# Kernel optimization log

Hardware: AMD Instinct MI355X
Metric: run time of the kernel (lower is better)

Reference implementation:

```python
import jax, jax.numpy as jnp
import numpy as np
from jax import lax

C = 16        # channel_n
HID = 128     # hidden_size
IC = 3        # input_channels (kept fixed each step)
STEPS = 32
FIRE_RATE = 0.5


def setup_inputs() -> dict:
    key = jax.random.key(0)
    k0, k1, k2, k3, k4 = jax.random.split(key, 5)
    B, H, W = 8, 256, 256
    x = jax.random.normal(k0, (B, C, H, W), jnp.float32)
    # depthwise 3x3 kernels, HWIO layout with I=1 (feature_group_count=C)
    w_p0 = jax.random.normal(k1, (3, 3, 1, C), jnp.float32) * 0.1
    w_p1 = jax.random.normal(k2, (3, 3, 1, C), jnp.float32) * 0.1
    # 1x1 conv MLP: fc0 [3C -> HID] (with bias), fc1 [HID -> C] (no bias)
    w_fc0 = jax.random.normal(k3, (3 * C, HID), jnp.float32) / np.sqrt(3.0 * C)
    b_fc0 = jnp.zeros((HID,), jnp.float32)
    # NOTE: original zero-inits fc1 (dx would be identically 0); use small
    # random weights so the baseline exercises nontrivial math.
    w_fc1 = jax.random.normal(k4, (HID, C), jnp.float32) * (0.1 / np.sqrt(HID))
    return {"x": x, "w_p0": w_p0, "w_p1": w_p1, "w_fc0": w_fc0,
            "b_fc0": b_fc0, "w_fc1": w_fc1}


def _dwconv3x3_reflect(x, w):
    # x: [B,H,W,C], w: [3,3,1,C]; reflect pad then depthwise VALID conv
    xp = jnp.pad(x, ((0, 0), (1, 1), (1, 1), (0, 0)), mode='reflect')
    return lax.conv_general_dilated(
        xp, w, window_strides=(1, 1), padding='VALID',
        dimension_numbers=('NHWC', 'HWIO', 'NHWC'), feature_group_count=C)


def reference(x, w_p0, w_p1, w_fc0, b_fc0, w_fc1):
    x = jnp.transpose(x, (0, 2, 3, 1))  # NCHW -> NHWC [B,H,W,C]
    img = x                              # input_image clone
    B, H, W, _ = x.shape
    keys = jax.random.split(jax.random.key(42), STEPS)

    def step(xc, k):
        perc = jnp.concatenate(
            [xc, _dwconv3x3_reflect(xc, w_p0), _dwconv3x3_reflect(xc, w_p1)],
            axis=-1)                                         # [B,H,W,3C]
        h = jax.nn.relu(jnp.einsum('bhwc,cd->bhwd', perc, w_fc0) + b_fc0)
        dx = jnp.einsum('bhwd,dc->bhwc', h, w_fc1)           # [B,H,W,C]
        mask = (jax.random.uniform(k, (B, H, W, 1)) <= FIRE_RATE).astype(xc.dtype)
        xn = xc + dx * mask
        # first IC channels hold the input image, kept fixed each step
        xn = jnp.concatenate([img[..., :IC], xn[..., IC:]], axis=-1)
        return xn, None

    x_final, _ = lax.scan(step, x, keys)
    x_final = jnp.transpose(x_final, (0, 3, 1, 2))  # NHWC -> NCHW
    out = x_final[:, 3:4, :, :]
    return out, x_final
```

## Files before the change

### kernel.cpp

```cpp
#include <hip/hip_runtime.h>
#include <stdint.h>

#define Cc   16
#define HIDD 128
#define Bn   8
#define Hh   256
#define Ww   256
#define HW   (Hh * Ww)
#define NPIX (Bn * HW)
#define NSTEPS 32

typedef _Float16 half8 __attribute__((ext_vector_type(8)));
typedef float floatx16 __attribute__((ext_vector_type(16)));

__host__ __device__ inline void threefry2x32(uint32_t k1, uint32_t k2,
                                             uint32_t x0, uint32_t x1,
                                             uint32_t& o0, uint32_t& o1) {
  const uint32_t ks2 = k1 ^ k2 ^ 0x1BD11BDAu;
  uint32_t v0 = x0 + k1;
  uint32_t v1 = x1 + k2;
#define ROTL32(x, n) (((x) << (n)) | ((x) >> (32 - (n))))
#define R4(a, b, c, d)                                    \
  { v0 += v1; v1 = ROTL32(v1, a); v1 ^= v0;               \
    v0 += v1; v1 = ROTL32(v1, b); v1 ^= v0;               \
    v0 += v1; v1 = ROTL32(v1, c); v1 ^= v0;               \
    v0 += v1; v1 = ROTL32(v1, d); v1 ^= v0; }
  R4(13, 15, 26, 6)   v0 += k2;  v1 += ks2 + 1u;
  R4(17, 29, 16, 24)  v0 += ks2; v1 += k1 + 2u;
  R4(13, 15, 26, 6)   v0 += k1;  v1 += k2 + 3u;
  R4(17, 29, 16, 24)  v0 += k2;  v1 += ks2 + 4u;
  R4(13, 15, 26, 6)   v0 += ks2; v1 += k1 + 5u;
#undef R4
#undef ROTL32
  o0 = v0;
  o1 = v1;
}

__device__ inline uint32_t pk2(_Float16 a, _Float16 b) {
  union { _Float16 h[2]; uint32_t u; } t;
  t.h[0] = a; t.h[1] = b;
  return t.u;
}
__device__ inline half8 mk8(uint32_t a, uint32_t b, uint32_t c, uint32_t d) {
  union { uint32_t u[4]; half8 h; } t;
  t.u[0] = a; t.u[1] = b; t.u[2] = c; t.u[3] = d;
  return t.h;
}

__global__ __launch_bounds__(256) void k_prep(const float* __restrict__ wfc0,
                                              const float* __restrict__ wfc1,
                                              unsigned short* __restrict__ wf) {
  const int idx = blockIdx.x * 256 + threadIdx.x;
  if (idx < 12288) {
    const int j = idx & 7;
    const int t = idx >> 3;
    const int lane = t & 63;
    const int t2 = t >> 6;
    const int spl = t2 & 1;
    const int fk = t2 >> 1;
    const int kt = fk % 3;
    const int Mt = fk / 3;
    const int m = Mt * 32 + (lane & 31);
    const int k = kt * 16 + (lane >> 5) * 8 + j;
    const float v = wfc0[k * HIDD + m];
    const _Float16 hi = (_Float16)v;
    const _Float16 r = spl ? (_Float16)(v - (float)hi) : hi;
    union { _Float16 h; unsigned short s; } cv; cv.h = r;
    wf[idx] = cv.s;
  } else if (idx < 20480) {
    const int idx2 = idx - 12288;
    const int j = idx2 & 7;
    const int t = idx2 >> 3;
    const int lane = t & 63;
    const int t2 = t >> 6;
    const int spl = t2 & 1;
    const int kt2 = t2 >> 1;
    const int m = lane & 31;
    const int k = kt2 * 16 + (lane >> 5) * 8 + j;
    const float v = (m < 13) ? wfc1[k * 16 + (m + 3)] : 0.f;
    const _Float16 hi = (_Float16)v;
    const _Float16 r = spl ? (_Float16)(v - (float)hi) : hi;
    union { _Float16 h; unsigned short s; } cv; cv.h = r;
    wf[idx] = cv.s;
  }
}

__global__ __launch_bounds__(256) void k_nchw_to_nhwc(const float* __restrict__ x,
                                                      float* __restrict__ st) {
  const int p = blockIdx.x * 256 + threadIdx.x;
  const int b = p >> 16;
  const int hw = p & 65535;
  const float* src = x + (size_t)b * (Cc * HW) + hw;
  float v[16];
#pragma unroll
  for (int c = 0; c < 16; c++) v[c] = src[(size_t)c * HW];
  float4* dst = (float4*)(st + (size_t)p * 16);
#pragma unroll
  for (int q = 0; q < 4; q++)
    dst[q] = make_float4(v[4 * q], v[4 * q + 1], v[4 * q + 2], v[4 * q + 3]);
}

__global__ __launch_bounds__(256) void k_step(const float* __restrict__ in,
                                              float* __restrict__ out,
                                              const float* __restrict__ wp0,
                                              const float* __restrict__ wp1,
                                              const unsigned short* __restrict__ wf,
                                              const float* __restrict__ bfc0,
                                              uint32_t key0, uint32_t key1) {
  __shared__ __align__(16) unsigned short s_wf[20480];
  __shared__ __align__(16) float s_bias[128];

  const int tid = threadIdx.x;
  {
    const uint4* src = (const uint4*)wf;
    uint4* dst = (uint4*)s_wf;
#pragma unroll
    for (int i = 0; i < 10; i++) dst[tid + 256 * i] = src[tid + 256 * i];
    if (tid < 32) ((float4*)s_bias)[tid] = ((const float4*)bfc0)[tid];
  }
  __syncthreads();

  const int lane = tid & 63;
  const int h8 = (tid >> 5) & 1;
  const int ln31 = tid & 31;
  const int wv = tid >> 6;
  const uint32_t wbase = ((uint32_t)blockIdx.x << 8) + (uint32_t)wv * 64u;

  const int b = blockIdx.x >> 8;
  const int h = blockIdx.x & 255;
  const int w = tid;
  const int rows[3] = { (h == 0) ? 1 : h - 1, h, (h == 255) ? 254 : h + 1 };
  const int cols[3] = { (w == 0) ? 1 : w - 1, w, (w == 255) ? 254 : w + 1 };

  float perc[48];
#pragma unroll
  for (int i = 16; i < 48; i++) perc[i] = 0.f;

#pragma unroll
  for (int ty = 0; ty < 3; ty++) {
#pragma unroll
    for (int tx = 0; tx < 3; tx++) {
      const int tap = ty * 3 + tx;
      const float4* pv =
          (const float4*)(in + (size_t)(((b << 8) + rows[ty]) * 256 + cols[tx]) * 16);
#pragma unroll
      for (int q = 0; q < 4; q++) {
        float4 v = pv[q];
        float vv[4] = { v.x, v.y, v.z, v.w };
#pragma unroll
        for (int j = 0; j < 4; j++) {
          const int c = 4 * q + j;
          perc[16 + c] = fmaf(wp0[tap * 16 + c], vv[j], perc[16 + c]);
          perc[32 + c] = fmaf(wp1[tap * 16 + c], vv[j], perc[32 + c]);
          if (tap == 4) perc[c] = vv[j];
        }
      }
    }
  }

  uint32_t hi2[24], lo2[24];
#pragma unroll
  for (int q = 0; q < 24; q++) {
    const float a = perc[2 * q], bq = perc[2 * q + 1];
    const _Float16 ah = (_Float16)a, bh = (_Float16)bq;
    const _Float16 al = (_Float16)(a - (float)ah), bl = (_Float16)(bq - (float)bh);
    hi2[q] = pk2(ah, bh);
    lo2[q] = pk2(al, bl);
  }

  uint32_t B0h[3][4], B0l[3][4], B1h[3][4], B1l[3][4];
#pragma unroll
  for (int kt = 0; kt < 3; kt++) {
#pragma unroll
    for (int d = 0; d < 4; d++) {
      const uint32_t olh = hi2[kt * 8 + d], ohh = hi2[kt * 8 + 4 + d];
      const uint32_t pl_h = __shfl_xor(olh, 32, 64);
      const uint32_t ph_h = __shfl_xor(ohh, 32, 64);
      B0h[kt][d] = h8 ? ph_h : olh;
      B1h[kt][d] = h8 ? ohh : pl_h;
      const uint32_t oll = lo2[kt * 8 + d], ohl = lo2[kt * 8 + 4 + d];
      const uint32_t pl_l = __shfl_xor(oll, 32, 64);
      const uint32_t ph_l = __shfl_xor(ohl, 32, 64);
      B0l[kt][d] = h8 ? ph_l : oll;
      B1l[kt][d] = h8 ? ohl : pl_l;
    }
  }

  floatx16 g2a, g2b;
#pragma unroll
  for (int i = 0; i < 16; i++) { g2a[i] = 0.f; g2b[i] = 0.f; }

#pragma unroll
  for (int Mt = 0; Mt < 4; Mt++) {
    half8 Ah[3], Al[3];
#pragma unroll
    for (int kt = 0; kt < 3; kt++) {
      Ah[kt] = *(const half8*)&s_wf[((Mt * 3 + kt) * 2 + 0) * 512 + lane * 8];
      Al[kt] = *(const half8*)&s_wf[((Mt * 3 + kt) * 2 + 1) * 512 + lane * 8];
    }
    const float4 bb0 = *(const float4*)&s_bias[Mt * 32 + 4 * h8];
    const float4 bb1 = *(const float4*)&s_bias[Mt * 32 + 8 + 4 * h8];
    const float4 bb2 = *(const float4*)&s_bias[Mt * 32 + 16 + 4 * h8];
    const float4 bb3 = *(const float4*)&s_bias[Mt * 32 + 24 + 4 * h8];
    floatx16 acc0 = { bb0.x, bb0.y, bb0.z, bb0.w, bb1.x, bb1.y, bb1.z, bb1.w,
                      bb2.x, bb2.y, bb2.z, bb2.w, bb3.x, bb3.y, bb3.z, bb3.w };
    floatx16 acc1 = acc0;

#pragma unroll
    for (int kt = 0; kt < 3; kt++) {
      const half8 b0h = mk8(B0h[kt][0], B0h[kt][1], B0h[kt][2], B0h[kt][3]);
      const half8 b0l = mk8(B0l[kt][0], B0l[kt][1], B0l[kt][2], B0l[kt][3]);
      const half8 b1h = mk8(B1h[kt][0], B1h[kt][1], B1h[kt][2], B1h[kt][3]);
      const half8 b1l = mk8(B1l[kt][0], B1l[kt][1], B1l[kt][2], B1l[kt][3]);
      acc0 = __builtin_amdgcn_mfma_f32_32x32x16_f16(Ah[kt], b0h, acc0, 0, 0, 0);
      acc0 = __builtin_amdgcn_mfma_f32_32x32x16_f16(Al[kt], b0h, acc0, 0, 0, 0);
      acc0 = __builtin_amdgcn_mfma_f32_32x32x16_f16(Ah[kt], b0l, acc0, 0, 0, 0);
      acc1 = __builtin_amdgcn_mfma_f32_32x32x16_f16(Ah[kt], b1h, acc1, 0, 0, 0);
      acc1 = __builtin_amdgcn_mfma_f32_32x32x16_f16(Al[kt], b1h, acc1, 0, 0, 0);
      acc1 = __builtin_amdgcn_mfma_f32_32x32x16_f16(Ah[kt], b1l, acc1, 0, 0, 0);
    }

#pragma unroll
    for (int u = 0; u < 2; u++) {
      const int kt2 = 2 * Mt + u;
      const half8 W1h = *(const half8*)&s_wf[12288 + (kt2 * 2 + 0) * 512 + lane * 8];
      const half8 W1l = *(const half8*)&s_wf[12288 + (kt2 * 2 + 1) * 512 + lane * 8];
#pragma unroll
      for (int nt = 0; nt < 2; nt++) {
        float hv[8];
#pragma unroll
        for (int s = 0; s < 8; s++) {
          const float v = nt ? acc1[8 * u + s] : acc0[8 * u + s];
          hv[s] = fmaxf(v, 0.f);
        }
        uint32_t pkh[4], pkl[4];
#pragma unroll
        for (int d = 0; d < 4; d++) {
          const float a = hv[2 * d], bq = hv[2 * d + 1];
          const _Float16 ah = (_Float16)a, bh = (_Float16)bq;
          const _Float16 al = (_Float16)(a - (float)ah), bl = (_Float16)(bq - (float)bh);
          pkh[d] = pk2(ah, bh);
          pkl[d] = pk2(al, bl);
        }
        uint32_t shh[4], shl[4];
#pragma unroll
        for (int d = 0; d < 4; d++) {
          shh[d] = __shfl_xor(pkh[d], 32, 64);
          shl[d] = __shfl_xor(pkl[d], 32, 64);
        }
        const half8 Bh2 = mk8(h8 ? shh[2] : pkh[0], h8 ? shh[3] : pkh[1],
                              h8 ? pkh[2] : shh[0], h8 ? pkh[3] : shh[1]);
        const half8 Bl2 = mk8(h8 ? shl[2] : pkl[0], h8 ? shl[3] : pkl[1],
                              h8 ? pkl[2] : shl[0], h8 ? pkl[3] : shl[1]);
        if (nt == 0) {
          g2a = __builtin_amdgcn_mfma_f32_32x32x16_f16(W1h, Bh2, g2a, 0, 0, 0);
          g2a = __builtin_amdgcn_mfma_f32_32x32x16_f16(W1l, Bh2, g2a, 0, 0, 0);
          g2a = __builtin_amdgcn_mfma_f32_32x32x16_f16(W1h, Bl2, g2a, 0, 0, 0);
        } else {
          g2b = __builtin_amdgcn_mfma_f32_32x32x16_f16(W1h, Bh2, g2b, 0, 0, 0);
          g2b = __builtin_amdgcn_mfma_f32_32x32x16_f16(W1l, Bh2, g2b, 0, 0, 0);
          g2b = __builtin_amdgcn_mfma_f32_32x32x16_f16(W1h, Bl2, g2b, 0, 0, 0);
        }
      }
    }
  }

#pragma unroll
  for (int nt = 0; nt < 2; nt++) {
    float dxv[8], odx[8];
#pragma unroll
    for (int i = 0; i < 8; i++) dxv[i] = nt ? g2b[i] : g2a[i];
#pragma unroll
    for (int i = 0; i < 8; i++) odx[i] = __shfl_xor(dxv[i], 32, 64);
    const uint32_t p = wbase + (uint32_t)(nt * 32) + (uint32_t)ln31;
    uint32_t t0, t1;
    threefry2x32(key0, key1, 0u, p, t0, t1);
    const uint32_t bits = t0 ^ t1;
    const float uu = __uint_as_float((bits >> 9) | 0x3f800000u) - 1.0f;
    const float M = (uu <= 0.5f) ? 1.f : 0.f;
    const float4* sp = (const float4*)(in + (size_t)p * 16);
    const float4 sA = sp[2 * h8];
    const float4 sB = sp[2 * h8 + 1];
    float4 oA, oB;
    oA.x = h8 ? fmaf(M, dxv[1], sA.x) : sA.x;
    oA.y = h8 ? fmaf(M, dxv[2], sA.y) : sA.y;
    oA.z = h8 ? fmaf(M, dxv[3], sA.z) : sA.z;
    oA.w = fmaf(M, h8 ? odx[4] : dxv[0], sA.w);
    oB.x = fmaf(M, h8 ? odx[5] : dxv[1], sB.x);
    oB.y = fmaf(M, h8 ? odx[6] : dxv[2], sB.y);
    oB.z = fmaf(M, h8 ? odx[7] : dxv[3], sB.z);
    oB.w = fmaf(M, h8 ? dxv[4] : odx[0], sB.w);
    float4* dp = (float4*)(out + (size_t)p * 16);
    dp[2 * h8] = oA;
    dp[2 * h8 + 1] = oB;
  }
}

__global__ __launch_bounds__(256) void k_nhwc_to_out(const float* __restrict__ st,
                                                     float* __restrict__ outp) {
  const int p = blockIdx.x * 256 + threadIdx.x;
  const int b = p >> 16;
  const int hw = p & 65535;
  const float4* src = (const float4*)(st + (size_t)p * 16);
  float v[16];
#pragma unroll
  for (int q = 0; q < 4; q++) {
    float4 t = src[q];
    v[4 * q] = t.x; v[4 * q + 1] = t.y; v[4 * q + 2] = t.z; v[4 * q + 3] = t.w;
  }
  float* xf = outp + NPIX;
#pragma unroll
  for (int c = 0; c < 16; c++) xf[(size_t)(b * 16 + c) * HW + hw] = v[c];
  outp[(size_t)b * HW + hw] = v[3];
}

extern "C" void kernel_launch(void* const* d_in, const int* in_sizes, int n_in,
                              void* d_out, int out_size, void* d_ws, size_t ws_size,
                              hipStream_t stream) {
  const float* x    = (const float*)d_in[0];
  const float* wp0  = (const float*)d_in[1];
  const float* wp1  = (const float*)d_in[2];
  const float* wfc0 = (const float*)d_in[3];
  const float* bfc0 = (const float*)d_in[4];
  const float* wfc1 = (const float*)d_in[5];
  float* out = (float*)d_out;

  unsigned short* wf = (unsigned short*)d_ws;
  float* S0 = (float*)((char*)d_ws + 65536);
  float* S1 = out + NPIX;

  uint32_t k0[NSTEPS], k1[NSTEPS];
  for (int s = 0; s < NSTEPS; s++)
    threefry2x32(0u, 42u, 0u, (uint32_t)s, k0[s], k1[s]);

  dim3 block(256);
  hipLaunchKernelGGL(k_prep, dim3(80), block, 0, stream, wfc0, wfc1, wf);
  hipLaunchKernelGGL(k_nchw_to_nhwc, dim3(NPIX / 256), block, 0, stream, x, S0);
  float* cur = S0;
  float* nxt = S1;
  for (int s = 0; s < NSTEPS; s++) {
    hipLaunchKernelGGL(k_step, dim3(Bn * Hh), block, 0, stream,
                       cur, nxt, wp0, wp1, wf, bfc0, k0[s], k1[s]);
    float* t = cur; cur = nxt; nxt = t;
  }
  hipLaunchKernelGGL(k_nhwc_to_out, dim3(NPIX / 256), block, 0, stream, cur, out);
}
```

Before: 1.849 ms.

## Permute weight rows to eliminate cross-lane shuffles; use permlane32 swap and block remap

The fc0 and fc1 weights are permuted at prep time so that the MFMA output layout of the hidden activations and of dx already matches the operand and store layouts. This removes the __shfl_xor exchanges between the two GEMMs and before the store. The remaining input-operand exchange uses v_permlane32_swap. The bias is now read from global memory instead of LDS, launch bounds request 4 blocks per SM, and blocks are remapped to interleave batches. The cost targeted is the LDS/ds_bpermute traffic from the shuffles; the risk is correctness of the hand-derived permutation.

```diff
diff --git a/kernel.cpp b/kernel.cpp
--- a/kernel.cpp
+++ b/kernel.cpp
@@ -47,6 +47,10 @@
   return t.h;
 }
 
+__device__ inline void pl32swap(uint32_t& a, uint32_t& b) {
+  asm("v_permlane32_swap_b32 %0, %1" : "+v"(a), "+v"(b));
+}
+
 __global__ __launch_bounds__(256) void k_prep(const float* __restrict__ wfc0,
                                               const float* __restrict__ wfc1,
                                               unsigned short* __restrict__ wf) {
@@ -60,9 +64,12 @@
     const int fk = t2 >> 1;
     const int kt = fk % 3;
     const int Mt = fk / 3;
-    const int m = Mt * 32 + (lane & 31);
+    const int rho = lane & 31;
+    const int r16 = rho & 15;
+    const int mlog = Mt * 32 + (rho >> 4) * 16
+                   + ((r16 >> 2) & 1) * 8 + ((r16 >> 3) & 1) * 4 + (r16 & 3);
     const int k = kt * 16 + (lane >> 5) * 8 + j;
-    const float v = wfc0[k * HIDD + m];
+    const float v = wfc0[k * HIDD + mlog];
     const _Float16 hi = (_Float16)v;
     const _Float16 r = spl ? (_Float16)(v - (float)hi) : hi;
     union { _Float16 h; unsigned short s; } cv; cv.h = r;
@@ -75,9 +82,14 @@
     const int t2 = t >> 6;
     const int spl = t2 & 1;
     const int kt2 = t2 >> 1;
-    const int m = lane & 31;
+    const int rho = lane & 31;
+    int ml = -1;
+    if (rho < 4) ml = rho;
+    else if (rho < 8) ml = rho + 1;
+    else if (rho == 8) ml = 4;
+    else if (rho >= 12 && rho < 16) ml = rho - 3;
     const int k = kt2 * 16 + (lane >> 5) * 8 + j;
-    const float v = (m < 13) ? wfc1[k * 16 + (m + 3)] : 0.f;
+    const float v = (ml >= 0) ? wfc1[k * 16 + (ml + 3)] : 0.f;
     const _Float16 hi = (_Float16)v;
     const _Float16 r = spl ? (_Float16)(v - (float)hi) : hi;
     union { _Float16 h; unsigned short s; } cv; cv.h = r;
@@ -100,15 +112,14 @@
     dst[q] = make_float4(v[4 * q], v[4 * q + 1], v[4 * q + 2], v[4 * q + 3]);
 }
 
-__global__ __launch_bounds__(256) void k_step(const float* __restrict__ in,
-                                              float* __restrict__ out,
-                                              const float* __restrict__ wp0,
-                                              const float* __restrict__ wp1,
-                                              const unsigned short* __restrict__ wf,
-                                              const float* __restrict__ bfc0,
-                                              uint32_t key0, uint32_t key1) {
+__global__ __launch_bounds__(256, 4) void k_step(const float* __restrict__ in,
+                                                 float* __restrict__ out,
+                                                 const float* __restrict__ wp0,
+                                                 const float* __restrict__ wp1,
+                                                 const unsigned short* __restrict__ wf,
+                                                 const float* __restrict__ bfc0,
+                                                 uint32_t key0, uint32_t key1) {
   __shared__ __align__(16) unsigned short s_wf[20480];
-  __shared__ __align__(16) float s_bias[128];
 
   const int tid = threadIdx.x;
   {
@@ -116,7 +127,6 @@
     uint4* dst = (uint4*)s_wf;
 #pragma unroll
     for (int i = 0; i < 10; i++) dst[tid + 256 * i] = src[tid + 256 * i];
-    if (tid < 32) ((float4*)s_bias)[tid] = ((const float4*)bfc0)[tid];
   }
   __syncthreads();
 
@@ -124,10 +134,12 @@
   const int h8 = (tid >> 5) & 1;
   const int ln31 = tid & 31;
   const int wv = tid >> 6;
-  const uint32_t wbase = ((uint32_t)blockIdx.x << 8) + (uint32_t)wv * 64u;
-
-  const int b = blockIdx.x >> 8;
-  const int h = blockIdx.x & 255;
+
+  const int bid = ((blockIdx.x & 7) << 8) | ((int)blockIdx.x >> 3);
+  const uint32_t wbase = ((uint32_t)bid << 8) + (uint32_t)wv * 64u;
+
+  const int b = bid >> 8;
+  const int h = bid & 255;
   const int w = tid;
   const int rows[3] = { (h == 0) ? 1 : h - 1, h, (h == 255) ? 254 : h + 1 };
   const int cols[3] = { (w == 0) ? 1 : w - 1, w, (w == 255) ? 254 : w + 1 };
@@ -173,22 +185,20 @@
   for (int kt = 0; kt < 3; kt++) {
 #pragma unroll
     for (int d = 0; d < 4; d++) {
-      const uint32_t olh = hi2[kt * 8 + d], ohh = hi2[kt * 8 + 4 + d];
-      const uint32_t pl_h = __shfl_xor(olh, 32, 64);
-      const uint32_t ph_h = __shfl_xor(ohh, 32, 64);
-      B0h[kt][d] = h8 ? ph_h : olh;
-      B1h[kt][d] = h8 ? ohh : pl_h;
-      const uint32_t oll = lo2[kt * 8 + d], ohl = lo2[kt * 8 + 4 + d];
-      const uint32_t pl_l = __shfl_xor(oll, 32, 64);
-      const uint32_t ph_l = __shfl_xor(ohl, 32, 64);
-      B0l[kt][d] = h8 ? ph_l : oll;
-      B1l[kt][d] = h8 ? ohl : pl_l;
+      uint32_t ah = hi2[kt * 8 + d], bh = hi2[kt * 8 + 4 + d];
+      pl32swap(ah, bh);
+      B0h[kt][d] = ah; B1h[kt][d] = bh;
+      uint32_t al = lo2[kt * 8 + d], bl = lo2[kt * 8 + 4 + d];
+      pl32swap(al, bl);
+      B0l[kt][d] = al; B1l[kt][d] = bl;
     }
   }
 
   floatx16 g2a, g2b;
 #pragma unroll
   for (int i = 0; i < 16; i++) { g2a[i] = 0.f; g2b[i] = 0.f; }
+
+  const float4* bp = (const float4*)bfc0;
 
 #pragma unroll
   for (int Mt = 0; Mt < 4; Mt++) {
@@ -198,10 +208,10 @@
       Ah[kt] = *(const half8*)&s_wf[((Mt * 3 + kt) * 2 + 0) * 512 + lane * 8];
       Al[kt] = *(const half8*)&s_wf[((Mt * 3 + kt) * 2 + 1) * 512 + lane * 8];
     }
-    const float4 bb0 = *(const float4*)&s_bias[Mt * 32 + 4 * h8];
-    const float4 bb1 = *(const float4*)&s_bias[Mt * 32 + 8 + 4 * h8];
-    const float4 bb2 = *(const float4*)&s_bias[Mt * 32 + 16 + 4 * h8];
-    const float4 bb3 = *(const float4*)&s_bias[Mt * 32 + 24 + 4 * h8];
+    const float4 bb0 = bp[Mt * 8 + 2 * h8];
+    const float4 bb1 = bp[Mt * 8 + 2 * h8 + 1];
+    const float4 bb2 = bp[Mt * 8 + 4 + 2 * h8];
+    const float4 bb3 = bp[Mt * 8 + 4 + 2 * h8 + 1];
     floatx16 acc0 = { bb0.x, bb0.y, bb0.z, bb0.w, bb1.x, bb1.y, bb1.z, bb1.w,
                       bb2.x, bb2.y, bb2.z, bb2.w, bb3.x, bb3.y, bb3.z, bb3.w };
     floatx16 acc1 = acc0;
@@ -242,16 +252,8 @@
           pkh[d] = pk2(ah, bh);
           pkl[d] = pk2(al, bl);
         }
-        uint32_t shh[4], shl[4];
-#pragma unroll
-        for (int d = 0; d < 4; d++) {
-          shh[d] = __shfl_xor(pkh[d], 32, 64);
-          shl[d] = __shfl_xor(pkl[d], 32, 64);
-        }
-        const half8 Bh2 = mk8(h8 ? shh[2] : pkh[0], h8 ? shh[3] : pkh[1],
-                              h8 ? pkh[2] : shh[0], h8 ? pkh[3] : shh[1]);
-        const half8 Bl2 = mk8(h8 ? shl[2] : pkl[0], h8 ? shl[3] : pkl[1],
-                              h8 ? pkl[2] : shl[0], h8 ? pkl[3] : shl[1]);
+        const half8 Bh2 = mk8(pkh[0], pkh[1], pkh[2], pkh[3]);
+        const half8 Bl2 = mk8(pkl[0], pkl[1], pkl[2], pkl[3]);
         if (nt == 0) {
           g2a = __builtin_amdgcn_mfma_f32_32x32x16_f16(W1h, Bh2, g2a, 0, 0, 0);
           g2a = __builtin_amdgcn_mfma_f32_32x32x16_f16(W1l, Bh2, g2a, 0, 0, 0);
@@ -267,11 +269,9 @@
 
 #pragma unroll
   for (int nt = 0; nt < 2; nt++) {
-    float dxv[8], odx[8];
+    float dxv[8];
 #pragma unroll
     for (int i = 0; i < 8; i++) dxv[i] = nt ? g2b[i] : g2a[i];
-#pragma unroll
-    for (int i = 0; i < 8; i++) odx[i] = __shfl_xor(dxv[i], 32, 64);
     const uint32_t p = wbase + (uint32_t)(nt * 32) + (uint32_t)ln31;
     uint32_t t0, t1;
     threefry2x32(key0, key1, 0u, p, t0, t1);
@@ -282,14 +282,14 @@
     const float4 sA = sp[2 * h8];
     const float4 sB = sp[2 * h8 + 1];
     float4 oA, oB;
-    oA.x = h8 ? fmaf(M, dxv[1], sA.x) : sA.x;
-    oA.y = h8 ? fmaf(M, dxv[2], sA.y) : sA.y;
-    oA.z = h8 ? fmaf(M, dxv[3], sA.z) : sA.z;
-    oA.w = fmaf(M, h8 ? odx[4] : dxv[0], sA.w);
-    oB.x = fmaf(M, h8 ? odx[5] : dxv[1], sB.x);
-    oB.y = fmaf(M, h8 ? odx[6] : dxv[2], sB.y);
-    oB.z = fmaf(M, h8 ? odx[7] : dxv[3], sB.z);
-    oB.w = fmaf(M, h8 ? dxv[4] : odx[0], sB.w);
+    oA.x = h8 ? fmaf(M, dxv[0], sA.x) : sA.x;
+    oA.y = h8 ? fmaf(M, dxv[1], sA.y) : sA.y;
+    oA.z = h8 ? fmaf(M, dxv[2], sA.z) : sA.z;
+    oA.w = fmaf(M, h8 ? dxv[3] : dxv[0], sA.w);
+    oB.x = fmaf(M, h8 ? dxv[4] : dxv[1], sB.x);
+    oB.y = fmaf(M, h8 ? dxv[5] : dxv[2], sB.y);
+    oB.z = fmaf(M, h8 ? dxv[6] : dxv[3], sB.z);
+    oB.w = fmaf(M, h8 ? dxv[7] : dxv[4], sB.w);
     float4* dp = (float4*)(out + (size_t)p * 16);
     dp[2 * h8] = oA;
     dp[2 * h8 + 1] = oB;
```

After: 1.911 ms. +3.4%, slower.
